# Kernel optimization log

Hardware: AMD Instinct MI355X
Metric: run time of the kernel (lower is better)

The kernel has to match this reference:

```python
import jax, jax.numpy as jnp
import numpy as np

B, H, S, D = 2, 16, 2048, 64  # depth = dmodel / num_heads
DMODEL = H * D


def setup_inputs() -> dict:
    key = jax.random.key(0)
    kq, kk, kv, kw = jax.random.split(key, 4)
    Q = jax.random.normal(kq, (B, H, S, D), dtype=jnp.float32)
    K = jax.random.normal(kk, (B, H, S, D), dtype=jnp.float32)
    V = jax.random.normal(kv, (B, H, S, D), dtype=jnp.float32)
    W = jax.random.normal(kw, (DMODEL, DMODEL), dtype=jnp.float32) * (1.0 / np.sqrt(DMODEL))
    b = jnp.zeros((DMODEL,), dtype=jnp.float32)
    return {"Q": Q, "K": K, "V": V, "W": W, "b": b}


def reference(Q, K, V, W, b):
    depth = Q.shape[-1]
    # scores: (B, H, S, S) -- full score matrix, matching the original math
    scores = jnp.einsum('bhqd,bhkd->bhqk', Q, K) / jnp.sqrt(jnp.float32(depth))
    attn = jax.nn.softmax(scores, axis=-1)
    vals = jnp.einsum('bhqk,bhkd->bhqd', attn, V)          # (B, H, S, D)
    vals = jnp.transpose(vals, (0, 2, 1, 3))               # (B, S, H, D)
    concat = vals.reshape(vals.shape[0], vals.shape[1], -1)  # (B, S, dmodel)
    return concat @ W + b
```

## Files before the change

### kernel.cpp

```cpp
#include <hip/hip_runtime.h>
#include <hip/hip_bf16.h>


typedef float  f32x16 __attribute__((ext_vector_type(16)));
typedef float  f32x4v __attribute__((ext_vector_type(4)));
typedef __bf16 bf16x8 __attribute__((ext_vector_type(8)));
typedef __bf16 bf16x4 __attribute__((ext_vector_type(4)));
typedef __bf16 bf16x2 __attribute__((ext_vector_type(2)));

static constexpr int Bn = 2, Hn = 16, Sn = 2048, Dn = 64, DM = 1024;
static constexpr size_t QKV_ELEMS = (size_t)Bn * Hn * Sn * Dn;
static constexpr int HD = Sn * Dn;

#define QSCALE 0.18033688011112042f

#if __has_builtin(__builtin_amdgcn_cvt_pk_bf16_f32)
static __device__ __forceinline__ unsigned pack2(float a, float b) {
  bf16x2 t = __builtin_amdgcn_cvt_pk_bf16_f32(a, b);
  union { bf16x2 v; unsigned u; } c; c.v = t; return c.u;
}
#else
static __device__ __forceinline__ unsigned pack2(float a, float b) {
  union { __bf16 h; unsigned short s; } ua, ub;
  ua.h = (__bf16)a; ub.h = (__bf16)b;
  return (unsigned)ua.s | ((unsigned)ub.s << 16);
}
#endif

static __device__ __forceinline__ void unzip8(const unsigned* wds, bf16x8* r0, bf16x8* r1) {
  union { unsigned u[4]; bf16x8 v; } a, b;
#pragma unroll
  for (int i = 0; i < 4; ++i) {
    unsigned lo = wds[2 * i], hi = wds[2 * i + 1];
    a.u[i] = (lo & 0xffffu) | (hi << 16);
    b.u[i] = (lo >> 16) | (hi & 0xffff0000u);
  }
  *r0 = a.v; *r1 = b.v;
}

__global__ __launch_bounds__(256) void convert_all(
    const float* __restrict__ k,
    const float* __restrict__ v, const float* __restrict__ w,
    __bf16* __restrict__ kf, __bf16* __restrict__ vf, __bf16* __restrict__ wt) {
  __shared__ __bf16 T[64][74];
  const int bid = blockIdx.x, t = threadIdx.x;

  if (bid < 256) {
    const int R = bid * 256 + t;
    const int bh = R >> 11, r = R & 2047;
    const int tt = r >> 5, ln = r & 31;
    const float* src = k + (size_t)R * Dn;
    __bf16* dst = kf + (size_t)bh * HD;
#pragma unroll
    for (int c = 0; c < 8; ++c) {
      f32x4v f0 = *(const f32x4v*)(src + c * 8);
      f32x4v f1 = *(const f32x4v*)(src + c * 8 + 4);
      bf16x8 o;
#pragma unroll
      for (int j = 0; j < 4; ++j) { o[j] = (__bf16)f0[j]; o[4 + j] = (__bf16)f1[j]; }
      const int ks = c >> 1, g = c & 1;
      *(bf16x8*)(dst + ((size_t)(tt * 4 + ks) * 64 + ln + 32 * g) * 8) = o;
    }
    return;
  }

  const int r = t >> 2, c0 = (t & 3) * 16;
  const float* s0;
  if (bid < 1280) {
    const int idx = bid - 256;
    const int kv0 = (idx & 31) * 64, bh = idx >> 5;
    s0 = v + ((size_t)bh * Sn + kv0 + r) * Dn + c0;
    union { bf16x8 v8; unsigned u[4]; } o0, o1;
#pragma unroll
    for (int i = 0; i < 2; ++i) {
      f32x4v f = *(const f32x4v*)(s0 + i * 4);
#pragma unroll
      for (int j = 0; j < 4; ++j) o0.v8[i * 4 + j] = (__bf16)f[j];
    }
#pragma unroll
    for (int i = 0; i < 2; ++i) {
      f32x4v f = *(const f32x4v*)(s0 + 8 + i * 4);
#pragma unroll
      for (int j = 0; j < 4; ++j) o1.v8[i * 4 + j] = (__bf16)f[j];
    }
#pragma unroll
    for (int j = 0; j < 4; ++j) {
      *(unsigned*)&T[r][c0 + 2 * j]     = o0.u[j];
      *(unsigned*)&T[r][c0 + 8 + 2 * j] = o1.u[j];
    }
    __syncthreads();
    const int rp = t >> 3, k0 = (t & 7) * 8;
    unsigned wds[8];
#pragma unroll
    for (int i = 0; i < 8; ++i) wds[i] = *(const unsigned*)&T[k0 + i][2 * rp];
    bf16x8 r0, r1; unzip8(wds, &r0, &r1);
    const int kvL = kv0 + k0;
    const int tt = (kvL >> 5) & 63, s4 = (kvL >> 4) & 1, jo = ((kvL >> 3) & 1) * 4;
    const int d0 = 2 * rp, half = d0 >> 5, lnd = d0 & 31;
    __bf16* vb = vf + (size_t)(idx >> 5) * HD +
                 (size_t)((tt * 2 + s4) * 2 + half) * 512;
    union { bf16x8 v8; bf16x4 h[2]; } a0, a1; a0.v8 = r0; a1.v8 = r1;
    *(bf16x4*)(vb + (lnd)*8 + jo)      = a0.h[0];
    *(bf16x4*)(vb + (lnd + 32) * 8 + jo) = a0.h[1];
    *(bf16x4*)(vb + (lnd + 1) * 8 + jo)  = a1.h[0];
    *(bf16x4*)(vb + (lnd + 33) * 8 + jo) = a1.h[1];
    return;
  }
  {
    const int idx = bid - 1280;
    const int nt = (idx & 15) * 64, kt = (idx >> 4) * 64;
    s0 = w + (size_t)(kt + r) * DM + nt + c0;
    union { bf16x8 v8; unsigned u[4]; } o0, o1;
#pragma unroll
    for (int i = 0; i < 2; ++i) {
      f32x4v f = *(const f32x4v*)(s0 + i * 4);
#pragma unroll
      for (int j = 0; j < 4; ++j) o0.v8[i * 4 + j] = (__bf16)f[j];
    }
#pragma unroll
    for (int i = 0; i < 2; ++i) {
      f32x4v f = *(const f32x4v*)(s0 + 8 + i * 4);
#pragma unroll
      for (int j = 0; j < 4; ++j) o1.v8[i * 4 + j] = (__bf16)f[j];
    }
#pragma unroll
    for (int j = 0; j < 4; ++j) {
      *(unsigned*)&T[r][c0 + 2 * j]     = o0.u[j];
      *(unsigned*)&T[r][c0 + 8 + 2 * j] = o1.u[j];
    }
    __syncthreads();
    const int rp = t >> 3, k0 = (t & 7) * 8;
    unsigned wds[8];
#pragma unroll
    for (int i = 0; i < 8; ++i) wds[i] = *(const unsigned*)&T[k0 + i][2 * rp];
    bf16x8 r0, r1; unzip8(wds, &r0, &r1);
    __bf16* d0 = wt + (size_t)(nt + 2 * rp) * DM + kt + k0;
    *(bf16x8*)d0 = r0;
    *(bf16x8*)(d0 + DM) = r1;
  }
}

__global__ __launch_bounds__(256, 2) void attn(
    const float* __restrict__ Qf, const __bf16* __restrict__ Kf,
    const __bf16* __restrict__ Vf, __bf16* __restrict__ Cc) {
  const int tid = threadIdx.x;
  const int wave = tid >> 6, lane = tid & 63;
  const int ln = lane & 31, g = lane >> 5;
  const int qb = blockIdx.x, h = blockIdx.y, bz = blockIdx.z;
  const int bh = bz * Hn + h;

  __shared__ __bf16 T[4][32][72];

  const float* Qp = Qf + (size_t)bh * HD + (size_t)(qb * 128 + wave * 32) * Dn;
  const __bf16* kbase = Kf + (size_t)bh * HD + (size_t)lane * 8;
  const __bf16* vbase = Vf + (size_t)bh * HD + (size_t)lane * 8;

  bf16x8 qf[4];
#pragma unroll
  for (int ks = 0; ks < 4; ++ks) {
    const float* qp = Qp + (size_t)ln * Dn + ks * 16 + g * 8;
    f32x4v f0 = *(const f32x4v*)qp;
    f32x4v f1 = *(const f32x4v*)(qp + 4);
#pragma unroll
    for (int j = 0; j < 4; ++j) {
      qf[ks][j]     = (__bf16)(f0[j] * QSCALE);
      qf[ks][4 + j] = (__bf16)(f1[j] * QSCALE);
    }
  }
  bf16x8 ones;
#pragma unroll
  for (int i = 0; i < 8; ++i) ones[i] = (__bf16)1.0f;

  f32x16 O0 = {}, O1 = {}, Ls = {};
  constexpr int NT = Sn / 32;

  bf16x8 kfr[2][4], vfr[2][4];
#pragma unroll
  for (int ks = 0; ks < 4; ++ks) kfr[0][ks] = *(const bf16x8*)(kbase + (size_t)ks * 512);
#pragma unroll
  for (int u = 0; u < 4; ++u)    vfr[0][u]  = *(const bf16x8*)(vbase + (size_t)u * 512);

#pragma unroll 2
  for (int kt = 0; kt < NT; ++kt) {
    const int cur = kt & 1, nxt = cur ^ 1;
    if (kt + 1 < NT) {
      const __bf16* kp = kbase + (size_t)(kt + 1) * 2048;
      const __bf16* vp = vbase + (size_t)(kt + 1) * 2048;
#pragma unroll
      for (int ks = 0; ks < 4; ++ks) kfr[nxt][ks] = *(const bf16x8*)(kp + (size_t)ks * 512);
#pragma unroll
      for (int u = 0; u < 4; ++u)    vfr[nxt][u]  = *(const bf16x8*)(vp + (size_t)u * 512);
    }

    f32x16 s = {};
#pragma unroll
    for (int ks = 0; ks < 4; ++ks)
      s = __builtin_amdgcn_mfma_f32_32x32x16_bf16(kfr[cur][ks], qf[ks], s, 0, 0, 0);
    unsigned w[8];
#pragma unroll
    for (int tt = 0; tt < 8; ++tt)
      w[tt] = pack2(__builtin_amdgcn_exp2f(s[2 * tt]),
                    __builtin_amdgcn_exp2f(s[2 * tt + 1]));

#pragma unroll
    for (int s4 = 0; s4 < 2; ++s4) {
      union { unsigned u[4]; bf16x8 v; } pu;
      pu.u[0] = w[s4 * 4 + 0];
      pu.u[1] = w[s4 * 4 + 1];
      pu.u[2] = w[s4 * 4 + 2];
      pu.u[3] = w[s4 * 4 + 3];
      O0 = __builtin_amdgcn_mfma_f32_32x32x16_bf16(vfr[cur][s4 * 2 + 0], pu.v, O0, 0, 0, 0);
      O1 = __builtin_amdgcn_mfma_f32_32x32x16_bf16(vfr[cur][s4 * 2 + 1], pu.v, O1, 0, 0, 0);
      Ls = __builtin_amdgcn_mfma_f32_32x32x16_bf16(ones, pu.v, Ls, 0, 0, 0);
    }
  }

  const float inv = 1.0f / Ls[0];
  __bf16* Tw = &T[wave][0][0];
#pragma unroll
  for (int dh = 0; dh < 2; ++dh) {
#pragma unroll
    for (int a = 0; a < 4; ++a) {
      const f32x16 O = dh ? O1 : O0;
      bf16x4 t4;
#pragma unroll
      for (int c = 0; c < 4; ++c) t4[c] = (__bf16)(O[4 * a + c] * inv);
      *(bf16x4*)(Tw + ln * 72 + dh * 32 + 8 * a + 4 * g) = t4;
    }
  }
  const int q0 = qb * 128 + wave * 32;
#pragma unroll
  for (int i = 0; i < 4; ++i) {
    const int rq = i * 8 + (lane >> 3);
    const int c8 = (lane & 7) * 8;
    bf16x8 o = *(const bf16x8*)(Tw + rq * 72 + c8);
    size_t base = (((size_t)bz * Sn + q0 + rq) * Hn + h) * Dn + c8;
    *(bf16x8*)&Cc[base] = o;
  }
}

__global__ __launch_bounds__(512, 2) void proj(
    const __bf16* __restrict__ A, const __bf16* __restrict__ Wt,
    const float* __restrict__ bias, float* __restrict__ out) {
  const int tid = threadIdx.x, wave = tid >> 6, lane = tid & 63;
  const int ln = lane & 31, g = lane >> 5;
  const int mq = wave >> 1, nh = wave & 1;
  const int bm = blockIdx.x, bn = blockIdx.y;
  __shared__ __bf16 As[2][128][72];
  __shared__ __bf16 Bs[2][64][72];
  const int ar = tid >> 2, ac = (tid & 3) * 16;
  const int rb = tid >> 3, cb = (tid & 7) * 8;
  f32x16 acc = {};
  const __bf16* Ap = A + (size_t)(bm * 128) * DM;
  const __bf16* Wp = Wt + (size_t)(bn * 64) * DM;

  bf16x8 a0, a1, b0;
  {
    const __bf16* ap = Ap + (size_t)ar * DM + ac;
    a0 = *(const bf16x8*)ap; a1 = *(const bf16x8*)(ap + 8);
    b0 = *(const bf16x8*)(Wp + (size_t)rb * DM + cb);
  }
  *(bf16x8*)&As[0][ar][ac]     = a0;
  *(bf16x8*)&As[0][ar][ac + 8] = a1;
  *(bf16x8*)&Bs[0][rb][cb]     = b0;
  {
    const __bf16* ap = Ap + (size_t)ar * DM + 64 + ac;
    a0 = *(const bf16x8*)ap; a1 = *(const bf16x8*)(ap + 8);
    b0 = *(const bf16x8*)(Wp + (size_t)rb * DM + 64 + cb);
  }
  __syncthreads();

  constexpr int KT = DM / 64;
  for (int kt = 0; kt < KT; ++kt) {
    const int buf = kt & 1;
#pragma unroll
    for (int ks = 0; ks < 4; ++ks) {
      bf16x8 af = *(const bf16x8*)&As[buf][mq * 32 + ln][ks * 16 + g * 8];
      bf16x8 wf = *(const bf16x8*)&Bs[buf][nh * 32 + ln][ks * 16 + g * 8];
      acc = __builtin_amdgcn_mfma_f32_32x32x16_bf16(af, wf, acc, 0, 0, 0);
    }
    if (kt + 1 < KT) {
      const int nb = buf ^ 1;
      *(bf16x8*)&As[nb][ar][ac]     = a0;
      *(bf16x8*)&As[nb][ar][ac + 8] = a1;
      *(bf16x8*)&Bs[nb][rb][cb]     = b0;
      if (kt + 2 < KT) {
        const __bf16* ap = Ap + (size_t)ar * DM + (kt + 2) * 64 + ac;
        a0 = *(const bf16x8*)ap; a1 = *(const bf16x8*)(ap + 8);
        b0 = *(const bf16x8*)(Wp + (size_t)rb * DM + (kt + 2) * 64 + cb);
      }
    }
    __syncthreads();
  }
  const float bv = bias[bn * 64 + nh * 32 + ln];
#pragma unroll
  for (int r = 0; r < 16; ++r) {
    int row = bm * 128 + mq * 32 + (r & 3) + 8 * (r >> 2) + 4 * g;
    out[(size_t)row * DM + bn * 64 + nh * 32 + ln] = acc[r] + bv;
  }
}

extern "C" void kernel_launch(void* const* d_in, const int* in_sizes, int n_in,
                              void* d_out, int out_size, void* d_ws, size_t ws_size,
                              hipStream_t stream) {
  const float* Q = (const float*)d_in[0];
  const float* K = (const float*)d_in[1];
  const float* V = (const float*)d_in[2];
  const float* W = (const float*)d_in[3];
  const float* b = (const float*)d_in[4];
  float* out = (float*)d_out;

  __bf16* ws  = (__bf16*)d_ws;
  __bf16* Kf  = ws;
  __bf16* Vf  = Kf + QKV_ELEMS;
  __bf16* Cc  = Vf + QKV_ELEMS;
  __bf16* Wt  = Cc + QKV_ELEMS;

  convert_all<<<dim3(1536, 1, 1), 256, 0, stream>>>(K, V, W, Kf, Vf, Wt);
  attn<<<dim3(Sn / 128, Hn, Bn), 256, 0, stream>>>(Q, Kf, Vf, Cc);
  proj<<<dim3(Bn * Sn / 128, DM / 64, 1), 512, 0, stream>>>(Cc, Wt, b, out);
}
```

Before: 164.1 us.

## Split KV range across wave pairs in attention and reduce partials via LDS

New measurement: 215.9 us. 31.5% more time.

```diff
diff --git a/kernel.cpp b/kernel.cpp
--- a/kernel.cpp
+++ b/kernel.cpp
@@ -100,7 +100,7 @@
     __bf16* vb = vf + (size_t)(idx >> 5) * HD +
                  (size_t)((tt * 2 + s4) * 2 + half) * 512;
     union { bf16x8 v8; bf16x4 h[2]; } a0, a1; a0.v8 = r0; a1.v8 = r1;
-    *(bf16x4*)(vb + (lnd)*8 + jo)      = a0.h[0];
+    *(bf16x4*)(vb + (lnd)*8 + jo)        = a0.h[0];
     *(bf16x4*)(vb + (lnd + 32) * 8 + jo) = a0.h[1];
     *(bf16x4*)(vb + (lnd + 1) * 8 + jo)  = a1.h[0];
     *(bf16x4*)(vb + (lnd + 33) * 8 + jo) = a1.h[1];
@@ -140,18 +140,19 @@
   }
 }
 
-__global__ __launch_bounds__(256, 2) void attn(
+__global__ __launch_bounds__(256, 4) void attn(
     const float* __restrict__ Qf, const __bf16* __restrict__ Kf,
     const __bf16* __restrict__ Vf, __bf16* __restrict__ Cc) {
   const int tid = threadIdx.x;
   const int wave = tid >> 6, lane = tid & 63;
   const int ln = lane & 31, g = lane >> 5;
+  const int qg = wave >> 1, kh = wave & 1;
   const int qb = blockIdx.x, h = blockIdx.y, bz = blockIdx.z;
   const int bh = bz * Hn + h;
 
-  __shared__ __bf16 T[4][32][72];
-
-  const float* Qp = Qf + (size_t)bh * HD + (size_t)(qb * 128 + wave * 32) * Dn;
+  __shared__ char pool[18432];
+
+  const float* Qp = Qf + (size_t)bh * HD + (size_t)(qb * 64 + qg * 32) * Dn;
   const __bf16* kbase = Kf + (size_t)bh * HD + (size_t)lane * 8;
   const __bf16* vbase = Vf + (size_t)bh * HD + (size_t)lane * 8;
 
@@ -172,20 +173,24 @@
   for (int i = 0; i < 8; ++i) ones[i] = (__bf16)1.0f;
 
   f32x16 O0 = {}, O1 = {}, Ls = {};
-  constexpr int NT = Sn / 32;
+  constexpr int NI = Sn / 64;
 
   bf16x8 kfr[2][4], vfr[2][4];
-#pragma unroll
-  for (int ks = 0; ks < 4; ++ks) kfr[0][ks] = *(const bf16x8*)(kbase + (size_t)ks * 512);
-#pragma unroll
-  for (int u = 0; u < 4; ++u)    vfr[0][u]  = *(const bf16x8*)(vbase + (size_t)u * 512);
+  {
+    const __bf16* kp = kbase + (size_t)kh * 2048;
+    const __bf16* vp = vbase + (size_t)kh * 2048;
+#pragma unroll
+    for (int ks = 0; ks < 4; ++ks) kfr[0][ks] = *(const bf16x8*)(kp + (size_t)ks * 512);
+#pragma unroll
+    for (int u = 0; u < 4; ++u)    vfr[0][u]  = *(const bf16x8*)(vp + (size_t)u * 512);
+  }
 
 #pragma unroll 2
-  for (int kt = 0; kt < NT; ++kt) {
-    const int cur = kt & 1, nxt = cur ^ 1;
-    if (kt + 1 < NT) {
-      const __bf16* kp = kbase + (size_t)(kt + 1) * 2048;
-      const __bf16* vp = vbase + (size_t)(kt + 1) * 2048;
+  for (int i = 0; i < NI; ++i) {
+    const int cur = i & 1, nxt = cur ^ 1;
+    if (i + 1 < NI) {
+      const __bf16* kp = kbase + (size_t)(kh + 2 * (i + 1)) * 2048;
+      const __bf16* vp = vbase + (size_t)(kh + 2 * (i + 1)) * 2048;
 #pragma unroll
       for (int ks = 0; ks < 4; ++ks) kfr[nxt][ks] = *(const bf16x8*)(kp + (size_t)ks * 512);
 #pragma unroll
@@ -215,25 +220,60 @@
     }
   }
 
-  const float inv = 1.0f / Ls[0];
-  __bf16* Tw = &T[wave][0][0];
-#pragma unroll
-  for (int dh = 0; dh < 2; ++dh) {
-#pragma unroll
-    for (int a = 0; a < 4; ++a) {
-      const f32x16 O = dh ? O1 : O0;
-      bf16x4 t4;
-#pragma unroll
-      for (int c = 0; c < 4; ++c) t4[c] = (__bf16)(O[4 * a + c] * inv);
-      *(bf16x4*)(Tw + ln * 72 + dh * 32 + 8 * a + 4 * g) = t4;
-    }
-  }
-  const int q0 = qb * 128 + wave * 32;
-#pragma unroll
-  for (int i = 0; i < 4; ++i) {
-    const int rq = i * 8 + (lane >> 3);
-    const int c8 = (lane & 7) * 8;
-    bf16x8 o = *(const bf16x8*)(Tw + rq * 72 + c8);
+  float* Ex = (float*)pool;
+  const int slot = (qg * 64 + lane) * 36;
+  if (kh == 1) {
+#pragma unroll
+    for (int i = 0; i < 4; ++i) {
+      f32x4v t = {O0[4 * i], O0[4 * i + 1], O0[4 * i + 2], O0[4 * i + 3]};
+      *(f32x4v*)&Ex[slot + 4 * i] = t;
+    }
+#pragma unroll
+    for (int i = 0; i < 4; ++i) {
+      f32x4v t = {O1[4 * i], O1[4 * i + 1], O1[4 * i + 2], O1[4 * i + 3]};
+      *(f32x4v*)&Ex[slot + 16 + 4 * i] = t;
+    }
+    Ex[slot + 32] = Ls[0];
+  }
+  __syncthreads();
+  float inv = 0.0f;
+  if (kh == 0) {
+#pragma unroll
+    for (int i = 0; i < 4; ++i) {
+      f32x4v t = *(const f32x4v*)&Ex[slot + 4 * i];
+#pragma unroll
+      for (int c = 0; c < 4; ++c) O0[4 * i + c] += t[c];
+    }
+#pragma unroll
+    for (int i = 0; i < 4; ++i) {
+      f32x4v t = *(const f32x4v*)&Ex[slot + 16 + 4 * i];
+#pragma unroll
+      for (int c = 0; c < 4; ++c) O1[4 * i + c] += t[c];
+    }
+    inv = 1.0f / (Ls[0] + Ex[slot + 32]);
+  }
+  __syncthreads();
+  __bf16* T = (__bf16*)pool;
+  if (kh == 0) {
+#pragma unroll
+    for (int dh = 0; dh < 2; ++dh) {
+#pragma unroll
+      for (int a = 0; a < 4; ++a) {
+        const f32x16 O = dh ? O1 : O0;
+        bf16x4 t4;
+#pragma unroll
+        for (int c = 0; c < 4; ++c) t4[c] = (__bf16)(O[4 * a + c] * inv);
+        *(bf16x4*)&T[(qg * 32 + ln) * 72 + dh * 32 + 8 * a + 4 * g] = t4;
+      }
+    }
+  }
+  __syncthreads();
+  const int q0 = qb * 64;
+#pragma unroll
+  for (int i = 0; i < 2; ++i) {
+    const int rq = i * 32 + (tid >> 3);
+    const int c8 = (tid & 7) * 8;
+    bf16x8 o = *(const bf16x8*)&T[rq * 72 + c8];
     size_t base = (((size_t)bz * Sn + q0 + rq) * Hn + h) * Dn + c8;
     *(bf16x8*)&Cc[base] = o;
   }
@@ -317,6 +357,6 @@
   __bf16* Wt  = Cc + QKV_ELEMS;
 
   convert_all<<<dim3(1536, 1, 1), 256, 0, stream>>>(K, V, W, Kf, Vf, Wt);
-  attn<<<dim3(Sn / 128, Hn, Bn), 256, 0, stream>>>(Q, Kf, Vf, Cc);
+  attn<<<dim3(Sn / 64, Hn, Bn), 256, 0, stream>>>(Q, Kf, Vf, Cc);
   proj<<<dim3(Bn * Sn / 128, DM / 64, 1), 512, 0, stream>>>(Cc, Wt, b, out);
 }
```
